# Optimization experiments

Hardware: AMD Instinct MI355X
Metric: run time of the kernel (lower is better)

## Reference

```python
import jax, jax.numpy as jnp
import numpy as np

IN_DIM = 128
HIDDEN = 256
OUT_DIM = 128
N_NODES = 100000
N_EDGES = 500000
N_MC = 2


def setup_inputs() -> dict:
    key = jax.random.key(0)
    k1, k2, k3, k4 = jax.random.split(key, 4)
    edge_index = jax.random.randint(k1, (2, N_EDGES), 0, N_NODES, dtype=jnp.int64)
    mc_embeddings = jax.random.normal(k2, (N_MC, N_NODES, IN_DIM), dtype=jnp.float32)
    # kaiming_normal for Linear1 (fan_in = 2*IN_DIM) and Linear2 (fan_in = HIDDEN)
    W1 = jax.random.normal(k3, (2 * IN_DIM, HIDDEN), dtype=jnp.float32) * np.sqrt(2.0 / (2 * IN_DIM))
    b1 = jnp.zeros((HIDDEN,), dtype=jnp.float32)
    W2 = jax.random.normal(k4, (HIDDEN, OUT_DIM), dtype=jnp.float32) * np.sqrt(2.0 / HIDDEN)
    b2 = jnp.zeros((OUT_DIM,), dtype=jnp.float32)
    return {"edge_index": edge_index, "mc_embeddings": mc_embeddings,
            "W1": W1, "b1": b1, "W2": W2, "b2": b2}


def reference(edge_index, mc_embeddings, W1, b1, W2, b2):
    # cat([x[src], x[dst]]) @ W1 == x[src] @ W1[:D] + x[dst] @ W1[D:]
    src, dst = edge_index[0], edge_index[1]
    W1a, W1b = W1[:IN_DIM], W1[IN_DIM:]  # [D, H] each

    def per_mc(x):  # x: [N, D]
        h = x[src] @ W1a + x[dst] @ W1b + b1          # [E, H]
        h = jax.nn.relu(h)
        return h @ W2 + b2                            # [E, out]

    return jax.vmap(per_mc)(mc_embeddings)           # [M, E, out]
```

## Files before the change

### kernel.cpp

```cpp
#include <hip/hip_runtime.h>
#include <hip/hip_bf16.h>

#define IN_DIM   128
#define HIDDEN   256
#define OUT_DIM  128
#define N_NODES  100000
#define N_EDGES  500000
#define N_ROWS   (2 * N_EDGES)

typedef __bf16 bf16x8  __attribute__((ext_vector_type(8)));
typedef float  f32x16  __attribute__((ext_vector_type(16)));

#define W1S_OFF 0
#define W2S_OFF 131072
#define XBF_OFF 196608

__global__ void prep_weights(const float* __restrict__ W1,
                             const float* __restrict__ W2,
                             unsigned char* __restrict__ ws) {
  int t = blockIdx.x * 256 + threadIdx.x;
  if (t < HIDDEN * HIDDEN) {
    int n = t & 255, k = t >> 8;
    __bf16 b = (__bf16)W1[k * HIDDEN + n];
    int byte = W1S_OFF + n * 512 + ((k * 2) ^ ((n & 7) << 4));
    *reinterpret_cast<__bf16*>(ws + byte) = b;
  } else {
    int t2 = t - HIDDEN * HIDDEN;
    if (t2 < HIDDEN * OUT_DIM) {
      int n = t2 & 127, k = t2 >> 7;
      __bf16 b = (__bf16)W2[k * OUT_DIM + n];
      int byte = W2S_OFF + n * 512 + ((k * 2) ^ ((n & 7) << 4));
      *reinterpret_cast<__bf16*>(ws + byte) = b;
    }
  }
}

__global__ __launch_bounds__(256)
void prep_x(const float* __restrict__ x, unsigned char* __restrict__ xbf) {
  long i = ((long)blockIdx.x * 256 + threadIdx.x) * 8;
  float4 f0 = *reinterpret_cast<const float4*>(x + i);
  float4 f1 = *reinterpret_cast<const float4*>(x + i + 4);
  bf16x8 a;
  a[0] = (__bf16)f0.x; a[1] = (__bf16)f0.y; a[2] = (__bf16)f0.z; a[3] = (__bf16)f0.w;
  a[4] = (__bf16)f1.x; a[5] = (__bf16)f1.y; a[6] = (__bf16)f1.z; a[7] = (__bf16)f1.w;
  *reinterpret_cast<bf16x8*>(xbf + i * 2) = a;
}

static __device__ __forceinline__ unsigned pack_bf16(float a, float b) {
  __bf16 x = (__bf16)a, y = (__bf16)b;
  unsigned short ux = __builtin_bit_cast(unsigned short, x);
  unsigned short uy = __builtin_bit_cast(unsigned short, y);
  return (unsigned)ux | ((unsigned)uy << 16);
}

static __device__ __forceinline__ void h_pack(const f32x16 acc,
                                              const float* __restrict__ b1c,
                                              int hi, bf16x8& oe, bf16x8& oo) {
  float4 bv0 = *reinterpret_cast<const float4*>(b1c + hi * 4);
  float4 bv1 = *reinterpret_cast<const float4*>(b1c + 8 + hi * 4);
  float4 bv2 = *reinterpret_cast<const float4*>(b1c + 16 + hi * 4);
  float4 bv3 = *reinterpret_cast<const float4*>(b1c + 24 + hi * 4);
  unsigned w0 = pack_bf16(fmaxf(acc[0] + bv0.x, 0.f),  fmaxf(acc[1] + bv0.y, 0.f));
  unsigned w1 = pack_bf16(fmaxf(acc[2] + bv0.z, 0.f),  fmaxf(acc[3] + bv0.w, 0.f));
  unsigned w2 = pack_bf16(fmaxf(acc[4] + bv1.x, 0.f),  fmaxf(acc[5] + bv1.y, 0.f));
  unsigned w3 = pack_bf16(fmaxf(acc[6] + bv1.z, 0.f),  fmaxf(acc[7] + bv1.w, 0.f));
  unsigned w4 = pack_bf16(fmaxf(acc[8] + bv2.x, 0.f),  fmaxf(acc[9] + bv2.y, 0.f));
  unsigned w5 = pack_bf16(fmaxf(acc[10] + bv2.z, 0.f), fmaxf(acc[11] + bv2.w, 0.f));
  unsigned w6 = pack_bf16(fmaxf(acc[12] + bv3.x, 0.f), fmaxf(acc[13] + bv3.y, 0.f));
  unsigned w7 = pack_bf16(fmaxf(acc[14] + bv3.z, 0.f), fmaxf(acc[15] + bv3.w, 0.f));
  asm("v_permlane32_swap_b32 %0, %1" : "+v"(w0), "+v"(w2));
  asm("v_permlane32_swap_b32 %0, %1" : "+v"(w1), "+v"(w3));
  asm("v_permlane32_swap_b32 %0, %1" : "+v"(w4), "+v"(w6));
  asm("v_permlane32_swap_b32 %0, %1" : "+v"(w5), "+v"(w7));
  uint4 fe; fe.x = w0; fe.y = w1; fe.z = w2; fe.w = w3;
  uint4 fo; fo.x = w4; fo.y = w5; fo.z = w6; fo.w = w7;
  oe = __builtin_bit_cast(bf16x8, fe);
  oo = __builtin_bit_cast(bf16x8, fo);
}

__global__ __launch_bounds__(128)
void edge_mlp(const int* __restrict__ eidx,
              const unsigned char* __restrict__ xbf,
              const float* __restrict__ b1,
              const float* __restrict__ b2,
              const unsigned char* __restrict__ ws,
              float* __restrict__ out) {
  __shared__ __align__(16) unsigned char wbuf[32768];

  const int tid  = threadIdx.x;
  const int wv   = tid >> 6;
  const int lane = tid & 63;
  const int el   = lane & 31;
  const int hi   = lane >> 5;

  const long base = (long)blockIdx.x * 64;
  const long gr   = base + wv * 32 + el;
  const int  mc   = (gr >= N_EDGES) ? 1 : 0;
  const int  e    = (int)(gr - (long)mc * N_EDGES);
  const int  sn   = eidx[e];
  const int  dn   = eidx[N_EDGES + e];
  const unsigned char* xsb = xbf + ((long)mc * N_NODES + sn) * 256;
  const unsigned char* xdb = xbf + ((long)mc * N_NODES + dn) * 256;

  bf16x8 a1[16];
#pragma unroll
  for (int s = 0; s < 16; ++s) {
    const unsigned char* p = (s < 8) ? (xsb + s * 32 + hi * 16)
                                     : (xdb + (s - 8) * 32 + hi * 16);
    a1[s] = *reinterpret_cast<const bf16x8*>(p);
  }

#define STAGE2(t)                                                              \
  do {                                                                         \
    const unsigned char* g_ = ws + (t) * 16384;                                \
    _Pragma("unroll")                                                          \
    for (int i_ = 0; i_ < 16; ++i_) {                                          \
      __builtin_amdgcn_global_load_lds(                                        \
          (const __attribute__((address_space(1))) unsigned int*)(g_ + i_ * 2048 + tid * 16), \
          (__attribute__((address_space(3))) unsigned int*)(&wbuf[i_ * 2048 + tid * 16]),     \
          16, 0, 0);                                                           \
    }                                                                          \
  } while (0)

  const int rowb = el * 512;
  const int swz  = (el & 7) << 4;

  bf16x8 a2[16];

#pragma unroll
  for (int p = 0; p < 4; ++p) {
    const int c0 = 2 * p;
    __syncthreads();
    STAGE2(c0);
    __syncthreads();
    f32x16 aA = {}, aB = {};
#pragma unroll
    for (int ks = 0; ks < 16; ++ks) {
      const int off = rowb + ((ks * 32 + hi * 16) ^ swz);
      bf16x8 wfA = *reinterpret_cast<const bf16x8*>(&wbuf[off]);
      bf16x8 wfB = *reinterpret_cast<const bf16x8*>(&wbuf[16384 + off]);
      aA = __builtin_amdgcn_mfma_f32_32x32x16_bf16(wfA, a1[ks], aA, 0, 0, 0);
      aB = __builtin_amdgcn_mfma_f32_32x32x16_bf16(wfB, a1[ks], aB, 0, 0, 0);
    }
    h_pack(aA, b1 + c0 * 32,      hi, a2[2 * c0],     a2[2 * c0 + 1]);
    h_pack(aB, b1 + c0 * 32 + 32, hi, a2[2 * c0 + 2], a2[2 * c0 + 3]);
  }

#pragma unroll
  for (int q = 0; q < 2; ++q) {
    const int oc0 = 2 * q;
    __syncthreads();
    STAGE2(8 + oc0);
    __syncthreads();
    f32x16 aA = {}, aB = {};
#pragma unroll
    for (int kk = 0; kk < 16; ++kk) {
      const int off = rowb + ((kk * 32 + hi * 16) ^ swz);
      bf16x8 wfA = *reinterpret_cast<const bf16x8*>(&wbuf[off]);
      bf16x8 wfB = *reinterpret_cast<const bf16x8*>(&wbuf[16384 + off]);
      aA = __builtin_amdgcn_mfma_f32_32x32x16_bf16(a2[kk], wfA, aA, 0, 0, 0);
      aB = __builtin_amdgcn_mfma_f32_32x32x16_bf16(a2[kk], wfB, aB, 0, 0, 0);
    }
    const long r0 = base + wv * 32;
    float bvA = b2[oc0 * 32 + el];
    float bvB = b2[oc0 * 32 + 32 + el];
#pragma unroll
    for (int reg = 0; reg < 16; ++reg) {
      int m = (reg & 3) + 8 * (reg >> 2) + 4 * hi;
      out[(r0 + m) * OUT_DIM + oc0 * 32 + el]      = aA[reg] + bvA;
      out[(r0 + m) * OUT_DIM + oc0 * 32 + 32 + el] = aB[reg] + bvB;
    }
  }
#undef STAGE2
}

extern "C" void kernel_launch(void* const* d_in, const int* in_sizes, int n_in,
                              void* d_out, int out_size, void* d_ws, size_t ws_size,
                              hipStream_t stream) {
  const int*   eidx = (const int*)d_in[0];
  const float* x    = (const float*)d_in[1];
  const float* b1   = (const float*)d_in[3];
  const float* b2   = (const float*)d_in[5];
  float* out = (float*)d_out;
  unsigned char* ws = (unsigned char*)d_ws;

  prep_weights<<<(HIDDEN * HIDDEN + HIDDEN * OUT_DIM) / 256, 256, 0, stream>>>(
      (const float*)d_in[2], (const float*)d_in[4], ws);

  prep_x<<<12500, 256, 0, stream>>>(x, ws + XBF_OFF);

  edge_mlp<<<N_ROWS / 64, 128, 0, stream>>>(eidx, ws + XBF_OFF, b1, b2, ws, out);
  (void)in_sizes; (void)n_in; (void)out_size; (void)ws_size;
}
```

Measured before the change: 329.9 us.

## Double-buffer weight tiles in LDS with async prefetch and fold biases into MFMA

Replaces the stage-then-sync weight loading, which used a full 32KB buffer, with a 12-step pipeline over two 16KB LDS buffers. The next-but-one tile is prefetched with global_load_lds and gated by explicit vmcnt waits and raw s_barrier, so loading overlaps with the MFMA work. Biases are now added through an extra rank-1 MFMA with a ones fragment in bf16 instead of separate vector adds. Each tile is split into even and odd accumulators to shorten MFMA dependency chains. The hand-tuned vmcnt counts are fragile, and rounding the bias to bf16 slightly changes numerics.

After: 364.6 us. 10.5% more time.

```diff
diff --git a/kernel.cpp b/kernel.cpp
--- a/kernel.cpp
+++ b/kernel.cpp
@@ -53,21 +53,16 @@
   return (unsigned)ux | ((unsigned)uy << 16);
 }
 
-static __device__ __forceinline__ void h_pack(const f32x16 acc,
-                                              const float* __restrict__ b1c,
-                                              int hi, bf16x8& oe, bf16x8& oo) {
-  float4 bv0 = *reinterpret_cast<const float4*>(b1c + hi * 4);
-  float4 bv1 = *reinterpret_cast<const float4*>(b1c + 8 + hi * 4);
-  float4 bv2 = *reinterpret_cast<const float4*>(b1c + 16 + hi * 4);
-  float4 bv3 = *reinterpret_cast<const float4*>(b1c + 24 + hi * 4);
-  unsigned w0 = pack_bf16(fmaxf(acc[0] + bv0.x, 0.f),  fmaxf(acc[1] + bv0.y, 0.f));
-  unsigned w1 = pack_bf16(fmaxf(acc[2] + bv0.z, 0.f),  fmaxf(acc[3] + bv0.w, 0.f));
-  unsigned w2 = pack_bf16(fmaxf(acc[4] + bv1.x, 0.f),  fmaxf(acc[5] + bv1.y, 0.f));
-  unsigned w3 = pack_bf16(fmaxf(acc[6] + bv1.z, 0.f),  fmaxf(acc[7] + bv1.w, 0.f));
-  unsigned w4 = pack_bf16(fmaxf(acc[8] + bv2.x, 0.f),  fmaxf(acc[9] + bv2.y, 0.f));
-  unsigned w5 = pack_bf16(fmaxf(acc[10] + bv2.z, 0.f), fmaxf(acc[11] + bv2.w, 0.f));
-  unsigned w6 = pack_bf16(fmaxf(acc[12] + bv3.x, 0.f), fmaxf(acc[13] + bv3.y, 0.f));
-  unsigned w7 = pack_bf16(fmaxf(acc[14] + bv3.z, 0.f), fmaxf(acc[15] + bv3.w, 0.f));
+static __device__ __forceinline__ void h_pack_nb(const f32x16 acc,
+                                                 bf16x8& oe, bf16x8& oo) {
+  unsigned w0 = pack_bf16(fmaxf(acc[0], 0.f),  fmaxf(acc[1], 0.f));
+  unsigned w1 = pack_bf16(fmaxf(acc[2], 0.f),  fmaxf(acc[3], 0.f));
+  unsigned w2 = pack_bf16(fmaxf(acc[4], 0.f),  fmaxf(acc[5], 0.f));
+  unsigned w3 = pack_bf16(fmaxf(acc[6], 0.f),  fmaxf(acc[7], 0.f));
+  unsigned w4 = pack_bf16(fmaxf(acc[8], 0.f),  fmaxf(acc[9], 0.f));
+  unsigned w5 = pack_bf16(fmaxf(acc[10], 0.f), fmaxf(acc[11], 0.f));
+  unsigned w6 = pack_bf16(fmaxf(acc[12], 0.f), fmaxf(acc[13], 0.f));
+  unsigned w7 = pack_bf16(fmaxf(acc[14], 0.f), fmaxf(acc[15], 0.f));
   asm("v_permlane32_swap_b32 %0, %1" : "+v"(w0), "+v"(w2));
   asm("v_permlane32_swap_b32 %0, %1" : "+v"(w1), "+v"(w3));
   asm("v_permlane32_swap_b32 %0, %1" : "+v"(w4), "+v"(w6));
@@ -85,7 +80,7 @@
               const float* __restrict__ b2,
               const unsigned char* __restrict__ ws,
               float* __restrict__ out) {
-  __shared__ __align__(16) unsigned char wbuf[32768];
+  __shared__ __align__(16) unsigned char wbuf[2][16384];
 
   const int tid  = threadIdx.x;
   const int wv   = tid >> 6;
@@ -102,6 +97,12 @@
   const unsigned char* xsb = xbf + ((long)mc * N_NODES + sn) * 256;
   const unsigned char* xdb = xbf + ((long)mc * N_NODES + dn) * 256;
 
+  float b1v[8], b2v[4];
+#pragma unroll
+  for (int c = 0; c < 8; ++c) b1v[c] = b1[c * 32 + el];
+#pragma unroll
+  for (int c = 0; c < 4; ++c) b2v[c] = b2[c * 32 + el];
+
   bf16x8 a1[16];
 #pragma unroll
   for (int s = 0; s < 16; ++s) {
@@ -109,69 +110,86 @@
                                      : (xdb + (s - 8) * 32 + hi * 16);
     a1[s] = *reinterpret_cast<const bf16x8*>(p);
   }
-
-#define STAGE2(t)                                                              \
+  asm volatile("" ::: "memory");
+
+#define STAGE(t, b)                                                            \
   do {                                                                         \
     const unsigned char* g_ = ws + (t) * 16384;                                \
     _Pragma("unroll")                                                          \
-    for (int i_ = 0; i_ < 16; ++i_) {                                          \
+    for (int i_ = 0; i_ < 8; ++i_) {                                           \
       __builtin_amdgcn_global_load_lds(                                        \
           (const __attribute__((address_space(1))) unsigned int*)(g_ + i_ * 2048 + tid * 16), \
-          (__attribute__((address_space(3))) unsigned int*)(&wbuf[i_ * 2048 + tid * 16]),     \
+          (__attribute__((address_space(3))) unsigned int*)(&wbuf[b][i_ * 2048 + tid * 16]),  \
           16, 0, 0);                                                           \
     }                                                                          \
   } while (0)
 
+  STAGE(0, 0);
+  asm volatile("" ::: "memory");
+  STAGE(1, 1);
+  asm volatile("" ::: "memory");
+
+  bf16x8 onefrag = {};
+  if (hi == 0) onefrag[0] = (__bf16)1.0f;
+
   const int rowb = el * 512;
   const int swz  = (el & 7) << 4;
-
   bf16x8 a2[16];
 
 #pragma unroll
-  for (int p = 0; p < 4; ++p) {
-    const int c0 = 2 * p;
-    __syncthreads();
-    STAGE2(c0);
-    __syncthreads();
-    f32x16 aA = {}, aB = {};
-#pragma unroll
-    for (int ks = 0; ks < 16; ++ks) {
-      const int off = rowb + ((ks * 32 + hi * 16) ^ swz);
-      bf16x8 wfA = *reinterpret_cast<const bf16x8*>(&wbuf[off]);
-      bf16x8 wfB = *reinterpret_cast<const bf16x8*>(&wbuf[16384 + off]);
-      aA = __builtin_amdgcn_mfma_f32_32x32x16_bf16(wfA, a1[ks], aA, 0, 0, 0);
-      aB = __builtin_amdgcn_mfma_f32_32x32x16_bf16(wfB, a1[ks], aB, 0, 0, 0);
+  for (int t = 0; t < 12; ++t) {
+    if (t <= 8)       asm volatile("s_waitcnt vmcnt(8)"  ::: "memory");
+    else if (t <= 10) asm volatile("s_waitcnt vmcnt(24)" ::: "memory");
+    else              asm volatile("s_waitcnt vmcnt(16)" ::: "memory");
+    __builtin_amdgcn_s_barrier();
+    asm volatile("" ::: "memory");
+
+    if (t < 8) {
+      f32x16 aE = {}, aO = {};
+      bf16x8 bfr = {};
+      if (hi == 0) bfr[0] = (__bf16)b1v[t];
+      aE = __builtin_amdgcn_mfma_f32_32x32x16_bf16(bfr, onefrag, aE, 0, 0, 0);
+#pragma unroll
+      for (int ks = 0; ks < 8; ++ks) {
+        const int offE = rowb + (((2 * ks) * 32 + hi * 16) ^ swz);
+        const int offO = rowb + (((2 * ks + 1) * 32 + hi * 16) ^ swz);
+        bf16x8 wE = *reinterpret_cast<const bf16x8*>(&wbuf[t & 1][offE]);
+        bf16x8 wO = *reinterpret_cast<const bf16x8*>(&wbuf[t & 1][offO]);
+        aE = __builtin_amdgcn_mfma_f32_32x32x16_bf16(wE, a1[2 * ks],     aE, 0, 0, 0);
+        aO = __builtin_amdgcn_mfma_f32_32x32x16_bf16(wO, a1[2 * ks + 1], aO, 0, 0, 0);
+      }
+      f32x16 acc = aE + aO;
+      h_pack_nb(acc, a2[2 * t], a2[2 * t + 1]);
+    } else {
+      const int u = t - 8;
+      f32x16 aE = {}, aO = {};
+      bf16x8 bfr = {};
+      if (hi == 0) bfr[0] = (__bf16)b2v[u];
+      aE = __builtin_amdgcn_mfma_f32_32x32x16_bf16(onefrag, bfr, aE, 0, 0, 0);
+#pragma unroll
+      for (int ks = 0; ks < 8; ++ks) {
+        const int offE = rowb + (((2 * ks) * 32 + hi * 16) ^ swz);
+        const int offO = rowb + (((2 * ks + 1) * 32 + hi * 16) ^ swz);
+        bf16x8 wE = *reinterpret_cast<const bf16x8*>(&wbuf[t & 1][offE]);
+        bf16x8 wO = *reinterpret_cast<const bf16x8*>(&wbuf[t & 1][offO]);
+        aE = __builtin_amdgcn_mfma_f32_32x32x16_bf16(a2[2 * ks],     wE, aE, 0, 0, 0);
+        aO = __builtin_amdgcn_mfma_f32_32x32x16_bf16(a2[2 * ks + 1], wO, aO, 0, 0, 0);
+      }
+      f32x16 acc = aE + aO;
+      const long r0 = base + wv * 32;
+#pragma unroll
+      for (int reg = 0; reg < 16; ++reg) {
+        int m = (reg & 3) + 8 * (reg >> 2) + 4 * hi;
+        out[(r0 + m) * OUT_DIM + u * 32 + el] = acc[reg];
+      }
     }
-    h_pack(aA, b1 + c0 * 32,      hi, a2[2 * c0],     a2[2 * c0 + 1]);
-    h_pack(aB, b1 + c0 * 32 + 32, hi, a2[2 * c0 + 2], a2[2 * c0 + 3]);
+
+    asm volatile("" ::: "memory");
+    __builtin_amdgcn_s_barrier();
+    asm volatile("" ::: "memory");
+    if (t + 2 < 12) STAGE(t + 2, t & 1);
   }
-
-#pragma unroll
-  for (int q = 0; q < 2; ++q) {
-    const int oc0 = 2 * q;
-    __syncthreads();
-    STAGE2(8 + oc0);
-    __syncthreads();
-    f32x16 aA = {}, aB = {};
-#pragma unroll
-    for (int kk = 0; kk < 16; ++kk) {
-      const int off = rowb + ((kk * 32 + hi * 16) ^ swz);
-      bf16x8 wfA = *reinterpret_cast<const bf16x8*>(&wbuf[off]);
-      bf16x8 wfB = *reinterpret_cast<const bf16x8*>(&wbuf[16384 + off]);
-      aA = __builtin_amdgcn_mfma_f32_32x32x16_bf16(a2[kk], wfA, aA, 0, 0, 0);
-      aB = __builtin_amdgcn_mfma_f32_32x32x16_bf16(a2[kk], wfB, aB, 0, 0, 0);
-    }
-    const long r0 = base + wv * 32;
-    float bvA = b2[oc0 * 32 + el];
-    float bvB = b2[oc0 * 32 + 32 + el];
-#pragma unroll
-    for (int reg = 0; reg < 16; ++reg) {
-      int m = (reg & 3) + 8 * (reg >> 2) + 4 * hi;
-      out[(r0 + m) * OUT_DIM + oc0 * 32 + el]      = aA[reg] + bvA;
-      out[(r0 + m) * OUT_DIM + oc0 * 32 + 32 + el] = aB[reg] + bvB;
-    }
-  }
-#undef STAGE2
+#undef STAGE
 }
 
 extern "C" void kernel_launch(void* const* d_in, const int* in_sizes, int n_in,
```

## Use 8-wave blocks staging 64KB weight chunks to amortize LDS loads

Applied to the files above, without the earlier changes.

The edge MLP block grows from 2 to 8 waves (256 rows), and each staging step now loads four 32-column weight tiles (64KB LDS) instead of two. This cuts the number of barrier and stage rounds and shares each weight load across more rows. Each output tile now uses a single chain split into even and odd K accumulators to break the MFMA dependency chain. The cost is much more LDS per block, which limits occupancy, plus clamped tail handling because the grid no longer divides evenly.

Result: slower. 359.7 us (+9.0%).

```diff
diff --git a/kernel.cpp b/kernel.cpp
--- a/kernel.cpp
+++ b/kernel.cpp
@@ -78,14 +78,14 @@
   oo = __builtin_bit_cast(bf16x8, fo);
 }
 
-__global__ __launch_bounds__(128)
+__global__ __launch_bounds__(512)
 void edge_mlp(const int* __restrict__ eidx,
               const unsigned char* __restrict__ xbf,
               const float* __restrict__ b1,
               const float* __restrict__ b2,
               const unsigned char* __restrict__ ws,
               float* __restrict__ out) {
-  __shared__ __align__(16) unsigned char wbuf[32768];
+  __shared__ __align__(16) unsigned char wl[65536];
 
   const int tid  = threadIdx.x;
   const int wv   = tid >> 6;
@@ -93,10 +93,13 @@
   const int el   = lane & 31;
   const int hi   = lane >> 5;
 
-  const long base = (long)blockIdx.x * 64;
-  const long gr   = base + wv * 32 + el;
-  const int  mc   = (gr >= N_EDGES) ? 1 : 0;
-  const int  e    = (int)(gr - (long)mc * N_EDGES);
+  const long base = (long)blockIdx.x * 256;
+  const long row0 = base + wv * 32;
+  const bool wvalid = row0 < N_ROWS;
+  const long gr   = row0 + el;
+  const long grc  = (gr < N_ROWS) ? gr : (N_ROWS - 1);
+  const int  mc   = (grc >= N_EDGES) ? 1 : 0;
+  const int  e    = (int)(grc - (long)mc * N_EDGES);
   const int  sn   = eidx[e];
   const int  dn   = eidx[N_EDGES + e];
   const unsigned char* xsb = xbf + ((long)mc * N_NODES + sn) * 256;
@@ -110,68 +113,74 @@
     a1[s] = *reinterpret_cast<const bf16x8*>(p);
   }
 
-#define STAGE2(t)                                                              \
+#define STAGE4(t0)                                                             \
   do {                                                                         \
-    const unsigned char* g_ = ws + (t) * 16384;                                \
+    const unsigned char* g_ = ws + (t0) * 16384;                               \
     _Pragma("unroll")                                                          \
-    for (int i_ = 0; i_ < 16; ++i_) {                                          \
+    for (int i_ = 0; i_ < 8; ++i_) {                                           \
       __builtin_amdgcn_global_load_lds(                                        \
-          (const __attribute__((address_space(1))) unsigned int*)(g_ + i_ * 2048 + tid * 16), \
-          (__attribute__((address_space(3))) unsigned int*)(&wbuf[i_ * 2048 + tid * 16]),     \
+          (const __attribute__((address_space(1))) unsigned int*)(g_ + i_ * 8192 + tid * 16), \
+          (__attribute__((address_space(3))) unsigned int*)(&wl[i_ * 8192 + tid * 16]),       \
           16, 0, 0);                                                           \
     }                                                                          \
   } while (0)
 
   const int rowb = el * 512;
   const int swz  = (el & 7) << 4;
-
   bf16x8 a2[16];
 
 #pragma unroll
-  for (int p = 0; p < 4; ++p) {
-    const int c0 = 2 * p;
+  for (int w = 0; w < 2; ++w) {
+    if (w) __syncthreads();
+    STAGE4(w * 4);
     __syncthreads();
-    STAGE2(c0);
-    __syncthreads();
-    f32x16 aA = {}, aB = {};
-#pragma unroll
-    for (int ks = 0; ks < 16; ++ks) {
-      const int off = rowb + ((ks * 32 + hi * 16) ^ swz);
-      bf16x8 wfA = *reinterpret_cast<const bf16x8*>(&wbuf[off]);
-      bf16x8 wfB = *reinterpret_cast<const bf16x8*>(&wbuf[16384 + off]);
-      aA = __builtin_amdgcn_mfma_f32_32x32x16_bf16(wfA, a1[ks], aA, 0, 0, 0);
-      aB = __builtin_amdgcn_mfma_f32_32x32x16_bf16(wfB, a1[ks], aB, 0, 0, 0);
-    }
-    h_pack(aA, b1 + c0 * 32,      hi, a2[2 * c0],     a2[2 * c0 + 1]);
-    h_pack(aB, b1 + c0 * 32 + 32, hi, a2[2 * c0 + 2], a2[2 * c0 + 3]);
-  }
-
-#pragma unroll
-  for (int q = 0; q < 2; ++q) {
-    const int oc0 = 2 * q;
-    __syncthreads();
-    STAGE2(8 + oc0);
-    __syncthreads();
-    f32x16 aA = {}, aB = {};
-#pragma unroll
-    for (int kk = 0; kk < 16; ++kk) {
-      const int off = rowb + ((kk * 32 + hi * 16) ^ swz);
-      bf16x8 wfA = *reinterpret_cast<const bf16x8*>(&wbuf[off]);
-      bf16x8 wfB = *reinterpret_cast<const bf16x8*>(&wbuf[16384 + off]);
-      aA = __builtin_amdgcn_mfma_f32_32x32x16_bf16(a2[kk], wfA, aA, 0, 0, 0);
-      aB = __builtin_amdgcn_mfma_f32_32x32x16_bf16(a2[kk], wfB, aB, 0, 0, 0);
-    }
-    const long r0 = base + wv * 32;
-    float bvA = b2[oc0 * 32 + el];
-    float bvB = b2[oc0 * 32 + 32 + el];
-#pragma unroll
-    for (int reg = 0; reg < 16; ++reg) {
-      int m = (reg & 3) + 8 * (reg >> 2) + 4 * hi;
-      out[(r0 + m) * OUT_DIM + oc0 * 32 + el]      = aA[reg] + bvA;
-      out[(r0 + m) * OUT_DIM + oc0 * 32 + 32 + el] = aB[reg] + bvB;
-    }
-  }
-#undef STAGE2
+#pragma unroll
+    for (int cl = 0; cl < 4; ++cl) {
+      const int cc = w * 4 + cl;
+      const unsigned char* cb = wl + cl * 16384;
+      f32x16 aE = {}, aO = {};
+#pragma unroll
+      for (int ks = 0; ks < 8; ++ks) {
+        const int offE = rowb + (((2 * ks) * 32 + hi * 16) ^ swz);
+        const int offO = rowb + (((2 * ks + 1) * 32 + hi * 16) ^ swz);
+        bf16x8 wE = *reinterpret_cast<const bf16x8*>(cb + offE);
+        bf16x8 wO = *reinterpret_cast<const bf16x8*>(cb + offO);
+        aE = __builtin_amdgcn_mfma_f32_32x32x16_bf16(wE, a1[2 * ks],     aE, 0, 0, 0);
+        aO = __builtin_amdgcn_mfma_f32_32x32x16_bf16(wO, a1[2 * ks + 1], aO, 0, 0, 0);
+      }
+      f32x16 acc = aE + aO;
+      h_pack(acc, b1 + cc * 32, hi, a2[2 * cc], a2[2 * cc + 1]);
+    }
+  }
+
+  __syncthreads();
+  STAGE4(8);
+  __syncthreads();
+#pragma unroll
+  for (int oc = 0; oc < 4; ++oc) {
+    const unsigned char* cb = wl + oc * 16384;
+    f32x16 aE = {}, aO = {};
+#pragma unroll
+    for (int ks = 0; ks < 8; ++ks) {
+      const int offE = rowb + (((2 * ks) * 32 + hi * 16) ^ swz);
+      const int offO = rowb + (((2 * ks + 1) * 32 + hi * 16) ^ swz);
+      bf16x8 wE = *reinterpret_cast<const bf16x8*>(cb + offE);
+      bf16x8 wO = *reinterpret_cast<const bf16x8*>(cb + offO);
+      aE = __builtin_amdgcn_mfma_f32_32x32x16_bf16(a2[2 * ks],     wE, aE, 0, 0, 0);
+      aO = __builtin_amdgcn_mfma_f32_32x32x16_bf16(a2[2 * ks + 1], wO, aO, 0, 0, 0);
+    }
+    if (wvalid) {
+      f32x16 acc = aE + aO;
+      float bvo = b2[oc * 32 + el];
+      const long r0 = base + wv * 32;
+#pragma unroll
+      for (int reg = 0; reg < 16; ++reg) {
+        int m = (reg & 3) + 8 * (reg >> 2) + 4 * hi;
+        out[(r0 + m) * OUT_DIM + oc * 32 + el] = acc[reg] + bvo;
+      }
+    }
+  }
+#undef STAGE4
 }
 
 extern "C" void kernel_launch(void* const* d_in, const int* in_sizes, int n_in,
@@ -189,6 +198,6 @@
 
   prep_x<<<12500, 256, 0, stream>>>(x, ws + XBF_OFF);
 
-  edge_mlp<<<N_ROWS / 64, 128, 0, stream>>>(eidx, ws + XBF_OFF, b1, b2, ws, out);
+  edge_mlp<<<(N_ROWS + 255) / 256, 512, 0, stream>>>(eidx, ws + XBF_OFF, b1, b2, ws, out);
   (void)in_sizes; (void)n_in; (void)out_size; (void)ws_size;
 }
```
